# Performance work log

Hardware: AMD Instinct MI355X
Metric: run time of the kernel (lower is better)

Reference implementation:

```python
import jax, jax.numpy as jnp
import numpy as np

jax.config.update("jax_enable_x64", True)  # original uses torch fp64 for the reciprocal trick

# --- GenericE layout constants ---
N = 32            # NUM_POSITIONS
D = 128           # per-position feature dim
F = N * D         # flattened dim
B = 8192          # batch
NIB_A, NIB_B = 0, 1
SLOT_DIVIDEND, SLOT_DIVISOR, SLOT_REMAINDER, SLOT_QUOTIENT = 2, 3, 4, 5
OP_START, OPCODE, BASE = 64, 3, 2
S = 60.0          # DIV_SCALE
SM_S = 60.0       # SOFTMAX1_SCALE
OP_FLAT = 0 * D + OP_START + OPCODE  # flat index of opcode channel at position 0


def _build_weights():
    # ClearDivSlotsFFN: hidden_dim = 4 slots * 2 units; bake_clear_pair wiring
    cW_up = np.zeros((8, F), np.float32)
    cW_gate = np.zeros((8, F), np.float32)
    cW_down = np.zeros((F, 8), np.float32)
    for i, slot in enumerate([SLOT_DIVIDEND, SLOT_DIVISOR, SLOT_REMAINDER, SLOT_QUOTIENT]):
        h = 2 * i
        # delta[slot] = -(1/S) * relu(S*op_w) * slot_val  -> clears slot when opcode active
        cW_up[h, OP_FLAT] = S
        cW_gate[h, slot] = 1.0
        cW_down[slot, h] = -1.0 / S
        # guard unit of the pair (zero down weight, mirrors gather's guard unit)
        cW_up[h + 1, OP_FLAT] = -S
        cW_gate[h + 1, slot] = -1.0
    # GatherScalarFFN: hidden_dim = N + 1; wiring straight from the source
    H = N + 1
    gW_up = np.zeros((H, F), np.float32)
    gW_gate = np.zeros((H, F), np.float32)
    gW_down = np.zeros((F, H), np.float32)
    dst = 0 * D + SLOT_DIVIDEND
    for i in range(N):
        gW_up[i, OP_FLAT] = S
        gW_gate[i, i * D + NIB_A] = float(BASE ** i)
        gW_down[dst, i] = 1.0 / S
    gW_up[N, OP_FLAT] = -S
    gW_gate[N, dst] = -1.0
    # gW_down[dst, N] = 0.0 (explicit in source)
    return (jnp.asarray(cW_up), jnp.asarray(cW_gate), jnp.asarray(cW_down),
            jnp.asarray(gW_up), jnp.asarray(gW_gate), jnp.asarray(gW_down))


def setup_inputs() -> dict:
    key = jax.random.key(0)
    x = jax.random.uniform(key, (B, N, D), dtype=jnp.float32)
    cW_up, cW_gate, cW_down, gW_up, gW_gate, gW_down = _build_weights()
    base_powers = jnp.asarray([float(BASE ** j) for j in range(N)], dtype=jnp.float64)
    return {"x": x, "cW_up": cW_up, "cW_gate": cW_gate, "cW_down": cW_down,
            "gW_up": gW_up, "gW_gate": gW_gate, "gW_down": gW_down,
            "base_powers": base_powers}


def _ffn_delta(xf, W_up, W_gate, W_down):
    # GenericFlattenedFFN residual delta: W_down @ (relu(W_up x) * (W_gate x))
    h = jax.nn.relu(xf @ W_up.T) * (xf @ W_gate.T)   # [B, H]
    return h @ W_down.T                               # [B, F]


def reference(x, cW_up, cW_gate, cW_down, gW_up, gW_gate, gW_down, base_powers):
    Bc, Nc, Dc = x.shape
    xf = x.reshape(Bc, Nc * Dc)
    # d1 + d2: the two FFN branches (each branch's forward is x + delta, so diff is delta)
    d12 = _ffn_delta(xf, cW_up, cW_gate, cW_down) + _ffn_delta(xf, gW_up, gW_gate, gW_down)
    # d3: Softmax1 reciprocal trick in fp64 (matching torch .double())
    op_w = x[:, 0, OP_START + OPCODE]                         # [B]
    d = x[:, :Nc, NIB_B].astype(jnp.float64)                  # [B, N]
    val = jnp.maximum(d * base_powers, 0.5)
    scores = jnp.where(d > 0.5, jnp.log(val), jnp.float64(-SM_S))
    mx = scores.max(axis=-1, keepdims=True)                   # [B, 1]
    sum_ex = jnp.exp(scores - mx).sum(axis=-1)                # [B]
    recip = jnp.exp(-mx[..., 0]) / jnp.maximum(sum_ex, 1e-30)
    out = x + d12.reshape(Bc, Nc, Dc)
    return out.at[:, 0, SLOT_QUOTIENT].add(op_w * recip.astype(x.dtype))
```

## Files before the change

kernel.cpp:

```cpp
#include <hip/hip_runtime.h>
#include <math.h>


#define DDIM 128
#define FDIM 4096

__global__ __launch_bounds__(256) void div_merged_kernel(
    const float* __restrict__ x, float* __restrict__ out) {
  const long long row = blockIdx.x;
  const float* __restrict__ xr = x + row * (long long)FDIM;
  float* __restrict__ orow = out + row * (long long)FDIM;
  const int t = threadIdx.x;

  __shared__ float s_fix[4];

  if (t < 64) {
    const int lane = t;
    const bool active = lane < 32;
    double score = -60.0;
    double p = 0.0;
    if (active) {
      const double pw = (double)(1ULL << lane);
      const float va = xr[lane * DDIM + 0];
      const float vb = xr[lane * DDIM + 1];
      p = (double)va * pw;
      const double d = (double)vb;
      score = (d > 0.5) ? log(fmax(d * pw, 0.5)) : -60.0;
    }
    double mx = score;
#pragma unroll
    for (int off = 1; off < 64; off <<= 1)
      mx = fmax(mx, __shfl_xor(mx, off));
    double ex = active ? exp(score - mx) : 0.0;
#pragma unroll
    for (int off = 1; off < 64; off <<= 1) {
      ex += __shfl_xor(ex, off);
      p  += __shfl_xor(p, off);
    }
    if (lane == 0) {
      const float op    = xr[67];
      const float r60   = fmaxf(60.0f * op, 0.0f);
      const float inv60 = (float)(1.0 / 60.0);
      const double recip = exp(-mx) / fmax(ex, 1e-30);
      const float Pf = (float)p;
      const float x2 = xr[2], x3 = xr[3], x4v = xr[4], x5 = xr[5];
      const float dc2 = -((r60 * x2) * inv60);
      const float dc3 = -((r60 * x3) * inv60);
      const float dc4 = -((r60 * x4v) * inv60);
      const float dc5 = -((r60 * x5) * inv60);
      const float dg2 = (r60 * Pf) * inv60;
      s_fix[0] = x2 + (dc2 + dg2);
      s_fix[1] = x3 + dc3;
      s_fix[2] = x4v + dc4;
      s_fix[3] = (x5 + dc5) + op * (float)recip;
    }
  }
  __syncthreads();

  const float4* __restrict__ x4 = (const float4*)xr;
  float4* __restrict__ o4 = (float4*)orow;
#pragma unroll
  for (int k = 0; k < 4; ++k) {
    const int idx = k * 256 + t;
    float4 v = x4[idx];
    if (idx == 0) {
      v.z = s_fix[0];
      v.w = s_fix[1];
    } else if (idx == 1) {
      v.x = s_fix[2];
      v.y = s_fix[3];
    }
    o4[idx] = v;
  }
}

extern "C" void kernel_launch(void* const* d_in, const int* in_sizes, int n_in,
                              void* d_out, int out_size, void* d_ws, size_t ws_size,
                              hipStream_t stream) {
  const float* x = (const float*)d_in[0];
  float* out = (float*)d_out;
  const int rows = in_sizes[0] / FDIM;
  div_merged_kernel<<<rows, 256, 0, stream>>>(x, out);
}
```

Before: 244.5 us.

## Load row once, replace log/exp softmax with direct sum, overlap stores

The row is now read into registers once. Position values are taken from those loaded vectors through shared memory, so the first wave no longer makes separate strided scalar loads. The fp64 log/max/exp softmax reciprocal is replaced by the equivalent 1/sum of the clamped d*2^i terms, with exp(-60) standing in for masked entries. Bulk stores are issued before the barrier so they overlap with the reduction. This depends on the algebraic identity holding across input ranges, and may lose precision or overflow differently than the max-shifted form.

```diff
diff --git a/kernel.cpp b/kernel.cpp
--- a/kernel.cpp
+++ b/kernel.cpp
@@ -2,75 +2,73 @@
 #include <math.h>
 
 
-#define DDIM 128
 #define FDIM 4096
 
 __global__ __launch_bounds__(256) void div_merged_kernel(
     const float* __restrict__ x, float* __restrict__ out) {
   const long long row = blockIdx.x;
-  const float* __restrict__ xr = x + row * (long long)FDIM;
-  float* __restrict__ orow = out + row * (long long)FDIM;
+  const float4* __restrict__ x4 = (const float4*)(x + row * (long long)FDIM);
+  float4* __restrict__ o4 = (float4*)(out + row * (long long)FDIM);
   const int t = threadIdx.x;
 
-  __shared__ float s_fix[4];
+  __shared__ float sa[32];
+  __shared__ float sd[32];
 
-  if (t < 64) {
-    const int lane = t;
-    const bool active = lane < 32;
-    double score = -60.0;
-    double p = 0.0;
-    if (active) {
-      const double pw = (double)(1ULL << lane);
-      const float va = xr[lane * DDIM + 0];
-      const float vb = xr[lane * DDIM + 1];
-      p = (double)va * pw;
-      const double d = (double)vb;
-      score = (d > 0.5) ? log(fmax(d * pw, 0.5)) : -60.0;
-    }
-    double mx = score;
-#pragma unroll
-    for (int off = 1; off < 64; off <<= 1)
-      mx = fmax(mx, __shfl_xor(mx, off));
-    double ex = active ? exp(score - mx) : 0.0;
-#pragma unroll
-    for (int off = 1; off < 64; off <<= 1) {
-      ex += __shfl_xor(ex, off);
-      p  += __shfl_xor(p, off);
-    }
-    if (lane == 0) {
-      const float op    = xr[67];
-      const float r60   = fmaxf(60.0f * op, 0.0f);
-      const float inv60 = (float)(1.0 / 60.0);
-      const double recip = exp(-mx) / fmax(ex, 1e-30);
-      const float Pf = (float)p;
-      const float x2 = xr[2], x3 = xr[3], x4v = xr[4], x5 = xr[5];
-      const float dc2 = -((r60 * x2) * inv60);
-      const float dc3 = -((r60 * x3) * inv60);
-      const float dc4 = -((r60 * x4v) * inv60);
-      const float dc5 = -((r60 * x5) * inv60);
-      const float dg2 = (r60 * Pf) * inv60;
-      s_fix[0] = x2 + (dc2 + dg2);
-      s_fix[1] = x3 + dc3;
-      s_fix[2] = x4v + dc4;
-      s_fix[3] = (x5 + dc5) + op * (float)recip;
-    }
+  float4 v0 = x4[t];
+  float4 v1 = x4[t + 256];
+  float4 v2 = x4[t + 512];
+  float4 v3 = x4[t + 768];
+
+  if ((t & 31) == 0) {
+    const int n0 = t >> 5;
+    sa[n0]      = v0.x;  sd[n0]      = v0.y;
+    sa[n0 + 8]  = v1.x;  sd[n0 + 8]  = v1.y;
+    sa[n0 + 16] = v2.x;  sd[n0 + 16] = v2.y;
+    sa[n0 + 24] = v3.x;  sd[n0 + 24] = v3.y;
   }
+
+  if (t >= 2) o4[t] = v0;
+  o4[t + 256] = v1;
+  o4[t + 512] = v2;
+  o4[t + 768] = v3;
+
   __syncthreads();
 
-  const float4* __restrict__ x4 = (const float4*)xr;
-  float4* __restrict__ o4 = (float4*)orow;
+  if (t < 32) {
+    const float op = __shfl(v0.w, 16);
+
+    const double pw = (double)(1ULL << t);
+    const double a  = (double)sa[t];
+    const double d  = (double)sd[t];
+    double p  = a * pw;
+    double ts = (d > 0.5) ? fmax(d * pw, 0.5)
+                          : 8.75651076269652e-27;
 #pragma unroll
-  for (int k = 0; k < 4; ++k) {
-    const int idx = k * 256 + t;
-    float4 v = x4[idx];
-    if (idx == 0) {
-      v.z = s_fix[0];
-      v.w = s_fix[1];
-    } else if (idx == 1) {
-      v.x = s_fix[2];
-      v.y = s_fix[3];
+    for (int off = 1; off < 32; off <<= 1) {
+      p  += __shfl_xor(p, off);
+      ts += __shfl_xor(ts, off);
     }
-    o4[idx] = v;
+    const float r60   = fmaxf(60.0f * op, 0.0f);
+    const float inv60 = (float)(1.0 / 60.0);
+    const float Pf    = (float)p;
+    const float recip = (float)(1.0 / ts);
+
+    if (t == 0) {
+      const float x2v = v0.z, x3v = v0.w;
+      const float dc2 = -((r60 * x2v) * inv60);
+      const float dc3 = -((r60 * x3v) * inv60);
+      const float dg2 = (r60 * Pf) * inv60;
+      v0.z = x2v + (dc2 + dg2);
+      v0.w = x3v + dc3;
+      o4[0] = v0;
+    } else if (t == 1) {
+      const float x4v = v0.x, x5v = v0.y;
+      const float dc4 = -((r60 * x4v) * inv60);
+      const float dc5 = -((r60 * x5v) * inv60);
+      v0.x = x4v + dc4;
+      v0.y = (x5v + dc5) + op * recip;
+      o4[1] = v0;
+    }
   }
 }
 
```

Result: no change. 240.9 us (-1.5%).
